# Kernel tuning notes

Hardware: AMD Instinct MI355X
Metric: run time of the kernel (lower is better)

## Reference

```python
import jax, jax.numpy as jnp
import numpy as np

HID, QLORA, NH = 5120, 1536, 128
NOPE, ROPE, KVLORA = 128, 64, 512
QHD = NOPE + ROPE  # 192
VHD = 128
SCALE = QHD ** (-0.5) * 0.707
EPS = 1e-6


def rmsnorm(x, w):
    xf = x.astype(jnp.float32)
    var = jnp.mean(xf * xf, axis=-1, keepdims=True)
    return (w * (xf * jax.lax.rsqrt(var + EPS))).astype(x.dtype)


def setup_inputs() -> dict:
    key = jax.random.key(0)
    ks = jax.random.split(key, 10)
    b, q, past = 2, 512, 512
    s = 0.02
    return {
        "hidden_states": jax.random.normal(ks[0], (b, q, HID), jnp.float32),
        "attention_mask": jnp.zeros((b, 1, q, past + q), jnp.float32),
        "past_key": jax.random.normal(ks[1], (b, NH, past, QHD), jnp.float32),
        "past_value": jax.random.normal(ks[2], (b, NH, past, VHD), jnp.float32),
        "w_q_a": jax.random.normal(ks[3], (QLORA, HID), jnp.float32) * s,
        "g_q_a": jnp.ones((QLORA,), jnp.float32),
        "w_q_b": jax.random.normal(ks[4], (NH * QHD, QLORA), jnp.float32) * s,
        "w_kv_a": jax.random.normal(ks[5], (KVLORA + ROPE, HID), jnp.float32) * s,
        "g_kv_a": jnp.ones((KVLORA,), jnp.float32),
        "w_kv_b": jax.random.normal(ks[6], (NH * (NOPE + VHD), KVLORA), jnp.float32) * s,
    }


def reference(hidden_states, attention_mask, past_key, past_value,
              w_q_a, g_q_a, w_q_b, w_kv_a, g_kv_a, w_kv_b):
    b, q_len, _ = hidden_states.shape
    # Q path: low-rank down-proj -> RMSNorm -> up-proj
    q = rmsnorm(hidden_states @ w_q_a.T, g_q_a) @ w_q_b.T
    q = q.reshape(b, q_len, NH, QHD).transpose(0, 2, 1, 3)  # [b,h,q,192]
    q_nope, q_pe = q[..., :NOPE], q[..., NOPE:]
    # KV path: joint down-proj, split latent / rope key
    ckv = hidden_states @ w_kv_a.T                          # [b,q,576]
    compressed_kv, k_pe = ckv[..., :KVLORA], ckv[..., KVLORA:]
    kv = rmsnorm(compressed_kv, g_kv_a) @ w_kv_b.T
    kv = kv.reshape(b, q_len, NH, NOPE + VHD).transpose(0, 2, 1, 3)
    k_nope, value_states = kv[..., :NOPE], kv[..., NOPE:]
    k_pe = k_pe.reshape(b, 1, q_len, ROPE)                  # shared across heads
    query_states = jnp.concatenate([q_nope, q_pe], axis=-1)
    key_states = jnp.concatenate(
        [k_nope, jnp.broadcast_to(k_pe, (b, NH, q_len, ROPE))], axis=-1)
    key_states = jnp.concatenate([past_key, key_states], axis=2)
    value_states = jnp.concatenate([past_value, value_states], axis=2)
    scores = jnp.einsum('bhqd,bhkd->bhqk', query_states, key_states) * SCALE
    scores = scores + attention_mask
    attn = jax.nn.softmax(scores.astype(jnp.float32), axis=-1).astype(query_states.dtype)
    attn_output = jnp.einsum('bhqk,bhkv->bhqv', attn, value_states)
    return attn_output, key_states, value_states
```

## Files before the change

kernel.cpp:

```cpp
#include <hip/hip_runtime.h>

#define NB    2
#define QLEN  512
#define HIDD  5120
#define QLORA 1536
#define NHEAD 128
#define QHD   192
#define VHD   128
#define KVTOT 1024

typedef float          f32x4   __attribute__((ext_vector_type(4)));
typedef __bf16         bf16x8  __attribute__((ext_vector_type(8)));
typedef unsigned short u16x8   __attribute__((ext_vector_type(8)));
typedef unsigned short u16x4   __attribute__((ext_vector_type(4)));

static __device__ __forceinline__ unsigned short f2bf(float f) {
  union { float f; unsigned u; } v; v.f = f;
  return (unsigned short)((v.u + 0x7fffu + ((v.u >> 16) & 1u)) >> 16);
}

static __device__ __forceinline__ void g2l16(const void* g, void* l) {
  __builtin_amdgcn_global_load_lds(
      (const __attribute__((address_space(1))) void*)g,
      (__attribute__((address_space(3))) void*)l, 16, 0, 0);
}

__global__ __launch_bounds__(256) void zero_pad_k(unsigned short* __restrict__ dst) {
  int i = blockIdx.x * 256 + threadIdx.x;
  u16x8 z = {0, 0, 0, 0, 0, 0, 0, 0};
  *(u16x8*)(dst + (long)i * 8) = z;
}

struct CvtArgs {
  const float* src[5];
  unsigned short* dst[5];
  int off[6];
};

__global__ __launch_bounds__(256) void cvt_all_k(CvtArgs a) {
  int b = blockIdx.x, s = 0;
  #pragma unroll
  for (int k = 0; k < 4; ++k) if (b >= a.off[k + 1]) s = k + 1;
  long lb = b - a.off[s];
  const float* in = a.src[s];
  unsigned short* out = a.dst[s];
  long base = lb * 1024 + threadIdx.x;
  #pragma unroll
  for (int k = 0; k < 4; ++k) {
    long i = base + k * 256;
    f32x4 v = *(const f32x4*)(in + i * 4);
    u16x4 o;
    o[0] = f2bf(v[0]); o[1] = f2bf(v[1]); o[2] = f2bf(v[2]); o[3] = f2bf(v[3]);
    *(u16x4*)(out + i * 4) = o;
  }
}

__global__ __launch_bounds__(256) void flags_k(const float* __restrict__ mask,
                                               int* __restrict__ flags) {
  int id = blockIdx.x;
  int b = id >> 6, qt = (id >> 4) & 3, kt = id & 15;
  const float* base = mask + (long)b * 524288 + (long)qt * 128 * 1024 + kt * 64;
  int t = threadIdx.x, w = t >> 6;
  unsigned acc = 0;
  #pragma unroll
  for (int i = 0; i < 32; ++i) {
    int e = i * 256 + t;
    int r = e >> 6, c = e & 63;
    union { float f; unsigned u; } v; v.f = base[(long)r * 1024 + c];
    acc |= v.u;
  }
  int any = __any(acc != 0);
  __shared__ int sf[4];
  if ((t & 63) == 0) sf[w] = any;
  __syncthreads();
  if (t == 0) flags[id] = sf[0] | sf[1] | sf[2] | sf[3];
}

__global__ __launch_bounds__(256, 4) void gemm_qa_ckv(const unsigned short* __restrict__ A,
                                                      const unsigned short* __restrict__ Bm,
                                                      float* __restrict__ part) {
  __shared__ __align__(16) unsigned short sA[128 * 64];
  __shared__ __align__(16) unsigned short sB[64 * 64];
  const int t = threadIdx.x, w = t >> 6, l = t & 63;
  const int l15 = l & 15, lh = l >> 4;
  const int swz7 = l15 & 7;
  const int id = blockIdx.x;
  const int xcd = id & 7, slot = id >> 3;
  const int pz = xcd + 8 * (slot >> 3);
  const int mb = slot & 7;
  if (pz >= 68) return;
  const int z = (pz >= 34) ? 1 : 0;
  const int nb = pz - z * 34;
  const unsigned short* Ab = A + (long)mb * 128 * HIDD;
  const unsigned short* Bb = Bm + (long)nb * 64 * HIDD;
  f32x4 acc[2][4];
  #pragma unroll
  for (int i = 0; i < 2; ++i)
    #pragma unroll
    for (int j = 0; j < 4; ++j)
      #pragma unroll
      for (int r = 0; r < 4; ++r) acc[i][j][r] = 0.f;

  const int k0 = z * 2560;
  for (int kt = k0; kt < k0 + 2560; kt += 64) {
    #pragma unroll
    for (int i2 = 0; i2 < 4; ++i2) {
      int n = i2 * 256 + t, r = n >> 3, c = (n & 7) ^ (r & 7);
      g2l16(Ab + (long)r * HIDD + kt + c * 8, (char*)sA + (i2 * 256 + w * 64) * 16);
    }
    #pragma unroll
    for (int i2 = 0; i2 < 2; ++i2) {
      int n = i2 * 256 + t, r = n >> 3, c = (n & 7) ^ (r & 7);
      g2l16(Bb + (long)r * HIDD + kt + c * 8, (char*)sB + (i2 * 256 + w * 64) * 16);
    }
    __syncthreads();
    #pragma unroll
    for (int ks = 0; ks < 2; ++ks) {
      bf16x8 af[2], bfr[4];
      #pragma unroll
      for (int i = 0; i < 2; ++i)
        af[i] = *(const bf16x8*)(sA + (w * 32 + i * 16 + l15) * 64 + ((ks * 4 + lh) ^ swz7) * 8);
      #pragma unroll
      for (int j = 0; j < 4; ++j)
        bfr[j] = *(const bf16x8*)(sB + (j * 16 + l15) * 64 + ((ks * 4 + lh) ^ swz7) * 8);
      #pragma unroll
      for (int i = 0; i < 2; ++i)
        #pragma unroll
        for (int j = 0; j < 4; ++j)
          acc[i][j] = __builtin_amdgcn_mfma_f32_16x16x32_bf16(af[i], bfr[j], acc[i][j], 0, 0, 0);
    }
    __syncthreads();
  }
  float* po = part + (long)z * 1024 * 2176;
  const int colbase = nb * 64;
  #pragma unroll
  for (int i = 0; i < 2; ++i)
    #pragma unroll
    for (int j = 0; j < 4; ++j) {
      const int col = colbase + j * 16 + l15;
      #pragma unroll
      for (int r4 = 0; r4 < 4; ++r4) {
        const long row = (long)mb * 128 + w * 32 + i * 16 + lh * 4 + r4;
        po[row * 2176 + col] = acc[i][j][r4];
      }
    }
}

__global__ __launch_bounds__(256) void post_a_k(const float* __restrict__ part,
                                                const float* __restrict__ gq,
                                                const float* __restrict__ gkv,
                                                unsigned short* __restrict__ qan,
                                                unsigned short* __restrict__ ckvn,
                                                float* __restrict__ kout,
                                                unsigned short* __restrict__ kb) {
  const long ZS = 1024L * 2176;
  int bid = blockIdx.x, t = threadIdx.x;
  if (bid >= 2048) {
    int row = bid - 2048;
    int j = t & 63, h0 = t >> 6;
    const float* p = part + (long)row * 2176 + 2048 + j;
    float v = p[0] + p[ZS];
    unsigned short vb = f2bf(v);
    long b_ = row >> 9, qi = row & 511;
    for (int h = h0; h < NHEAD; h += 4) {
      long idx = ((b_ * NHEAD + h) * KVTOT + 512 + qi) * QHD + 128 + j;
      kout[idx] = v;
      kb[idx] = vb;
    }
    return;
  }
  bool isQ = bid < 1024;
  int row = isQ ? bid : bid - 1024;
  int cols = isQ ? 1536 : 512;
  const float* g = isQ ? gq : gkv;
  unsigned short* out = isQ ? (qan + (long)row * 1536) : (ckvn + (long)row * 512);
  const float* x = part + (long)row * 2176 + (isQ ? 0 : 1536);
  int w = t >> 6, l = t & 63;
  float xv[6];
  int nc = cols >> 8;
  float ss = 0.f;
  for (int i = 0; i < nc; ++i) {
    int c = t + i * 256;
    float v = x[c] + x[c + ZS];
    xv[i] = v; ss += v * v;
  }
  #pragma unroll
  for (int m = 32; m >= 1; m >>= 1) ss += __shfl_xor(ss, m);
  __shared__ float red[4];
  if (l == 0) red[w] = ss;
  __syncthreads();
  float tot = red[0] + red[1] + red[2] + red[3];
  float rs = rsqrtf(tot / (float)cols + 1e-6f);
  for (int i = 0; i < nc; ++i) {
    int c = t + i * 256;
    out[c] = f2bf(g[c] * xv[i] * rs);
  }
}

__global__ __launch_bounds__(256, 4) void gemm_bt2(const unsigned short* __restrict__ Aq,
                                                   const unsigned short* __restrict__ Bq,
                                                   const unsigned short* __restrict__ Akv,
                                                   const unsigned short* __restrict__ Bkv,
                                                   unsigned short* __restrict__ qout,
                                                   float* __restrict__ kout,
                                                   float* __restrict__ vout,
                                                   unsigned short* __restrict__ kb,
                                                   unsigned short* __restrict__ vt) {
  __shared__ __align__(16) unsigned short sA[128 * 64];
  __shared__ __align__(16) unsigned short sB[128 * 64];
  const int t = threadIdx.x, w = t >> 6, l = t & 63;
  const int l15 = l & 15, lh = l >> 4;
  const int swz7 = l15 & 7;
  const int wm = w >> 1, wn = w & 1;
  const int id = blockIdx.x;
  const int xcd = id & 7, slot = id >> 3;
  const int y = xcd + 8 * (slot >> 3);
  const int mb = slot & 7;
  const bool isQ = y < 192;
  const int nb = isQ ? y : y - 192;
  const int K = isQ ? QLORA : 512;
  const unsigned short* Ab = (isQ ? Aq : Akv) + (long)mb * 128 * K;
  const unsigned short* Bb = (isQ ? Bq : Bkv) + (long)nb * 128 * K;
  f32x4 acc[4][4];
  #pragma unroll
  for (int i = 0; i < 4; ++i)
    #pragma unroll
    for (int j = 0; j < 4; ++j)
      #pragma unroll
      for (int r = 0; r < 4; ++r) acc[i][j][r] = 0.f;

  const int srow = l >> 3;
  const int scol = ((l & 7) ^ srow) * 8;

  for (int kt = 0; kt < K; kt += 64) {
    #pragma unroll
    for (int i = 0; i < 4; ++i) {
      const int chunk = i * 4 + w;
      const int r = chunk * 8 + srow;
      g2l16(Ab + (long)r * K + kt + scol, (char*)sA + chunk * 1024);
      g2l16(Bb + (long)r * K + kt + scol, (char*)sB + chunk * 1024);
    }
    __syncthreads();
    #pragma unroll
    for (int ks = 0; ks < 2; ++ks) {
      bf16x8 af[4], bfr[4];
      #pragma unroll
      for (int i = 0; i < 4; ++i)
        af[i] = *(const bf16x8*)(sA + (wm * 64 + i * 16 + l15) * 64 + ((ks * 4 + lh) ^ swz7) * 8);
      #pragma unroll
      for (int j = 0; j < 4; ++j)
        bfr[j] = *(const bf16x8*)(sB + (wn * 64 + j * 16 + l15) * 64 + ((ks * 4 + lh) ^ swz7) * 8);
      #pragma unroll
      for (int i = 0; i < 4; ++i)
        #pragma unroll
        for (int j = 0; j < 4; ++j)
          acc[i][j] = __builtin_amdgcn_mfma_f32_16x16x32_bf16(af[i], bfr[j], acc[i][j], 0, 0, 0);
    }
    __syncthreads();
  }

  const long rowbase = (long)mb * 128 + wm * 64;
  const long b_ = rowbase >> 9;
  const int colbase = nb * 128 + wn * 64;
  #pragma unroll
  for (int i = 0; i < 4; ++i) {
    const long qi0 = (rowbase + i * 16 + lh * 4) & 511;
    #pragma unroll
    for (int j = 0; j < 4; ++j) {
      const int col = colbase + j * 16 + l15;
      if (isQ) {
        const int h = col / QHD, d = col - h * QHD;
        unsigned short* qp = qout + ((b_ * NHEAD + h) * QLEN + qi0) * QHD + d;
        #pragma unroll
        for (int r4 = 0; r4 < 4; ++r4) qp[(long)r4 * QHD] = f2bf(acc[i][j][r4]);
      } else {
        const int h = col >> 8, d = col & 255;
        if (d < 128) {
          const long idx = ((b_ * NHEAD + h) * KVTOT + 512 + qi0) * QHD + d;
          #pragma unroll
          for (int r4 = 0; r4 < 4; ++r4) {
            kout[idx + (long)r4 * QHD] = acc[i][j][r4];
            kb[idx + (long)r4 * QHD] = f2bf(acc[i][j][r4]);
          }
        } else {
          const int dv = d - 128;
          float* vp = vout + ((b_ * NHEAD + h) * KVTOT + 512 + qi0) * VHD + dv;
          u16x4 tv;
          #pragma unroll
          for (int r4 = 0; r4 < 4; ++r4) {
            vp[(long)r4 * VHD] = acc[i][j][r4];
            tv[r4] = f2bf(acc[i][j][r4]);
          }
          *(u16x4*)(vt + ((b_ * NHEAD + h) * VHD + dv) * KVTOT + 512 + qi0) = tv;
        }
      }
    }
  }
}

__global__ __launch_bounds__(256) void copy_key_past_k(const float* __restrict__ pk,
                                                       float* __restrict__ kout,
                                                       unsigned short* __restrict__ kb) {
  long i4 = (long)blockIdx.x * 256 + threadIdx.x;
  f32x4 v = *(const f32x4*)(pk + i4 * 4);
  long e = i4 * 4;
  long bh = e / 98304;
  long rem = e - bh * 98304;
  long oidx = bh * 196608 + rem;
  *(f32x4*)(kout + oidx) = v;
  u16x4 b;
  b[0] = f2bf(v[0]); b[1] = f2bf(v[1]); b[2] = f2bf(v[2]); b[3] = f2bf(v[3]);
  *(u16x4*)(kb + oidx) = b;
}

__global__ __launch_bounds__(256) void vfix_k(const float* __restrict__ pv,
                                              float* __restrict__ outv,
                                              unsigned short* __restrict__ vt) {
  __shared__ __align__(16) unsigned short sT[128 * 72];
  int bh = blockIdx.x >> 3, kt = blockIdx.x & 7;
  int t = threadIdx.x;
  const float* src = pv + ((long)bh * 512 + kt * 64) * VHD;
  float* dstv = outv + ((long)bh * KVTOT + kt * 64) * VHD;
  #pragma unroll
  for (int i = 0; i < 8; ++i) {
    int id = t + i * 256;
    int r = id >> 5, c4 = (id & 31) * 4;
    f32x4 v = *(const f32x4*)(src + (long)r * VHD + c4);
    *(f32x4*)(dstv + (long)r * VHD + c4) = v;
    #pragma unroll
    for (int jj = 0; jj < 4; ++jj) sT[(c4 + jj) * 72 + r] = f2bf(v[jj]);
  }
  __syncthreads();
  #pragma unroll
  for (int i = 0; i < 4; ++i) {
    int id = t + i * 256;
    int d = id >> 3, c = id & 7;
    u16x8 v = *(const u16x8*)(sT + d * 72 + c * 8);
    *(u16x8*)(vt + ((long)bh * VHD + d) * KVTOT + kt * 64 + c * 8) = v;
  }
}

static __device__ __forceinline__ void stage_k_tile(const unsigned short* __restrict__ src,
                                                    char* dstbase, int t) {
  const int w = t >> 6;
  #pragma unroll
  for (int i2 = 0; i2 < 6; ++i2) {
    int n = i2 * 256 + t;
    int r = n / 24, cp = n - r * 24;
    int c = cp ^ (r & 7);
    g2l16(src + (long)r * QHD + c * 8, dstbase + (i2 * 256 + w * 64) * 16);
  }
}

static __device__ __forceinline__ void stage_v_tile(const unsigned short* __restrict__ src,
                                                    char* dstbase, int t) {
  const int w = t >> 6;
  #pragma unroll
  for (int i2 = 0; i2 < 4; ++i2) {
    int n = i2 * 256 + t;
    int r = n >> 3, cp = n & 7;
    int c = cp ^ (r & 7);
    g2l16(src + (long)r * KVTOT + c * 8, dstbase + (i2 * 256 + w * 64) * 16);
  }
}

__global__ __launch_bounds__(256, 2) void attn_k(const unsigned short* __restrict__ Qw,
                                                 const unsigned short* __restrict__ Kb,
                                                 const unsigned short* __restrict__ Vt,
                                                 const float* __restrict__ mask,
                                                 const int* __restrict__ flags,
                                                 float* __restrict__ outp) {
  __shared__ __align__(16) unsigned short sK[64 * 192];
  __shared__ __align__(16) unsigned short sV[128 * 64];
  const int t = threadIdx.x, w = t >> 6, l = t & 63;
  const int l15 = l & 15, lh = l >> 4;
  const int raw = blockIdx.x;
  const int xcd = raw & 7, slot = raw >> 3;
  const int bh = xcd * 32 + (slot >> 2), qt = slot & 3;
  const long b_ = bh >> 7;
  const float SCALE = 0.051023330039633184f;
  const int swz = l15 & 7;

  bf16x8 qf[2][6];
  const unsigned short* Qb = Qw + ((long)bh * QLEN + qt * 128 + w * 32) * QHD;
  #pragma unroll
  for (int i = 0; i < 2; ++i)
    #pragma unroll
    for (int ks = 0; ks < 6; ++ks)
      qf[i][ks] = *(const bf16x8*)(Qb + (i * 16 + l15) * QHD + ks * 32 + lh * 8);

  f32x4 o[2][8];
  #pragma unroll
  for (int i = 0; i < 2; ++i)
    #pragma unroll
    for (int j = 0; j < 8; ++j)
      #pragma unroll
      for (int r = 0; r < 4; ++r) o[i][j][r] = 0.f;
  float m_[2][4], l_[2][4];
  #pragma unroll
  for (int i = 0; i < 2; ++i)
    #pragma unroll
    for (int r = 0; r < 4; ++r) { m_[i][r] = -1e30f; l_[i][r] = 0.f; }

  const int qrow0 = qt * 128 + w * 32;
  const unsigned short* Kbh = Kb + (long)bh * KVTOT * QHD;
  const unsigned short* Vbh = Vt + (long)bh * VHD * KVTOT;
  const float* mrow = mask + b_ * 524288 + (long)(qrow0 + lh * 4) * 1024 + l15;
  const int fbase = (int)b_ * 64 + qt * 16;

  for (int kt = 0; kt < 16; ++kt) {
    stage_k_tile(Kbh + (long)kt * 64 * QHD, (char*)sK, t);
    stage_v_tile(Vbh + kt * 64, (char*)sV, t);
    const int flag = flags[fbase + kt];
    __syncthreads();

    f32x4 s[2][4];
    #pragma unroll
    for (int i = 0; i < 2; ++i)
      #pragma unroll
      for (int j = 0; j < 4; ++j)
        #pragma unroll
        for (int r = 0; r < 4; ++r) s[i][j][r] = 0.f;
    __builtin_amdgcn_s_setprio(1);
    #pragma unroll
    for (int j = 0; j < 4; ++j) {
      #pragma unroll
      for (int ks = 0; ks < 6; ++ks) {
        bf16x8 kf = *(const bf16x8*)(sK + ((j * 16 + l15) * 24 + ((ks * 4 + lh) ^ swz)) * 8);
        s[0][j] = __builtin_amdgcn_mfma_f32_16x16x32_bf16(qf[0][ks], kf, s[0][j], 0, 0, 0);
        s[1][j] = __builtin_amdgcn_mfma_f32_16x16x32_bf16(qf[1][ks], kf, s[1][j], 0, 0, 0);
      }
    }
    __builtin_amdgcn_s_setprio(0);

    unsigned short pk16[2][4][4];
    #pragma unroll
    for (int i = 0; i < 2; ++i) {
      #pragma unroll
      for (int rg = 0; rg < 4; ++rg) {
        float sc[4];
        if (flag) {
          #pragma unroll
          for (int j = 0; j < 4; ++j)
            sc[j] = s[i][j][rg] * SCALE + mrow[(long)(i * 16 + rg) * 1024 + kt * 64 + j * 16];
        } else {
          #pragma unroll
          for (int j = 0; j < 4; ++j) sc[j] = s[i][j][rg] * SCALE;
        }
        float mx = fmaxf(fmaxf(sc[0], sc[1]), fmaxf(sc[2], sc[3]));
        mx = fmaxf(mx, __shfl_xor(mx, 1));
        mx = fmaxf(mx, __shfl_xor(mx, 2));
        mx = fmaxf(mx, __shfl_xor(mx, 4));
        mx = fmaxf(mx, __shfl_xor(mx, 8));
        float mo = m_[i][rg];
        float mn = fmaxf(mo, mx);
        if (__any(mn > mo)) {
          float al = __expf(mo - mn);
          #pragma unroll
          for (int jj = 0; jj < 8; ++jj) o[i][jj][rg] *= al;
          l_[i][rg] *= al;
          m_[i][rg] = mn;
        }
        float ps = 0.f;
        #pragma unroll
        for (int j = 0; j < 4; ++j) {
          float p = __expf(sc[j] - m_[i][rg]);
          ps += p;
          pk16[i][rg][j] = f2bf(p);
        }
        l_[i][rg] += ps;
      }
    }
    __syncthreads();

    unsigned short* sPc = (unsigned short*)sK;
    #pragma unroll
    for (int i = 0; i < 2; ++i)
      #pragma unroll
      for (int rg = 0; rg < 4; ++rg) {
        const int prow = w * 32 + i * 16 + lh * 4 + rg;
        #pragma unroll
        for (int j = 0; j < 4; ++j)
          sPc[prow * 72 + j * 16 + l15] = pk16[i][rg][j];
      }

    __builtin_amdgcn_s_setprio(1);
    #pragma unroll
    for (int ks = 0; ks < 2; ++ks) {
      bf16x8 pf0 = *(const bf16x8*)(sPc + (w * 32 + l15) * 72 + ks * 32 + lh * 8);
      bf16x8 pf1 = *(const bf16x8*)(sPc + (w * 32 + 16 + l15) * 72 + ks * 32 + lh * 8);
      #pragma unroll
      for (int jj = 0; jj < 8; ++jj) {
        bf16x8 vf = *(const bf16x8*)(sV + ((jj * 16 + l15) * 8 + ((ks * 4 + lh) ^ swz)) * 8);
        o[0][jj] = __builtin_amdgcn_mfma_f32_16x16x32_bf16(pf0, vf, o[0][jj], 0, 0, 0);
        o[1][jj] = __builtin_amdgcn_mfma_f32_16x16x32_bf16(pf1, vf, o[1][jj], 0, 0, 0);
      }
    }
    __builtin_amdgcn_s_setprio(0);
    __syncthreads();
  }

  #pragma unroll
  for (int i = 0; i < 2; ++i) {
    #pragma unroll
    for (int rg = 0; rg < 4; ++rg) {
      float ls = l_[i][rg];
      ls += __shfl_xor(ls, 1);
      ls += __shfl_xor(ls, 2);
      ls += __shfl_xor(ls, 4);
      ls += __shfl_xor(ls, 8);
      float inv = 1.0f / ls;
      long row = (long)bh * QLEN + qrow0 + i * 16 + lh * 4 + rg;
      #pragma unroll
      for (int jj = 0; jj < 8; ++jj)
        outp[row * VHD + jj * 16 + l15] = o[i][jj][rg] * inv;
    }
  }
}

#define WS_HID_BF   0L
#define WS_WQA_BF   10485760L
#define WS_WQB_BF   32768000L
#define WS_WKVB_BF  108265472L
#define WS_QAN_BF   141819904L
#define WS_CKVN_BF  144965632L
#define WS_Q_BF     146014208L
#define WS_KB_BF    196345856L
#define WS_VT_BF    297009152L
#define WS_FLAGS    364118016L

extern "C" void kernel_launch(void* const* d_in, const int* in_sizes, int n_in,
                              void* d_out, int out_size, void* d_ws, size_t ws_size,
                              hipStream_t stream) {
  const float* hs   = (const float*)d_in[0];
  const float* mask = (const float*)d_in[1];
  const float* pk   = (const float*)d_in[2];
  const float* pv   = (const float*)d_in[3];
  const float* wqa  = (const float*)d_in[4];
  const float* gqa  = (const float*)d_in[5];
  const float* wqb  = (const float*)d_in[6];
  const float* wkva = (const float*)d_in[7];
  const float* gkva = (const float*)d_in[8];
  const float* wkvb = (const float*)d_in[9];

  char* ws = (char*)d_ws;
  unsigned short* hid_bf  = (unsigned short*)(ws + WS_HID_BF);
  unsigned short* wqa_bf  = (unsigned short*)(ws + WS_WQA_BF);
  unsigned short* wkva_bf = wqa_bf + (long)1536 * 5120;
  unsigned short* wpad_bf = wqa_bf + (long)2112 * 5120;
  unsigned short* wqb_bf  = (unsigned short*)(ws + WS_WQB_BF);
  unsigned short* wkvb_bf = (unsigned short*)(ws + WS_WKVB_BF);
  unsigned short* qan_bf  = (unsigned short*)(ws + WS_QAN_BF);
  unsigned short* ckvn_bf = (unsigned short*)(ws + WS_CKVN_BF);
  unsigned short* q_bf    = (unsigned short*)(ws + WS_Q_BF);
  float*          part    = (float*)(ws + WS_Q_BF);
  unsigned short* kb_bf   = (unsigned short*)(ws + WS_KB_BF);
  unsigned short* vt_bf   = (unsigned short*)(ws + WS_VT_BF);
  int*            flags   = (int*)(ws + WS_FLAGS);

  float* out_attn = (float*)d_out;
  float* out_key  = (float*)d_out + 16777216;
  float* out_val  = (float*)d_out + 67108864;

  flags_k<<<128, 256, 0, stream>>>(mask, flags);
  zero_pad_k<<<160, 256, 0, stream>>>(wpad_bf);
  CvtArgs ca;
  ca.src[0] = hs;     ca.dst[0] = hid_bf;
  ca.src[1] = wqa;    ca.dst[1] = wqa_bf;
  ca.src[2] = wkva;   ca.dst[2] = wkva_bf;
  ca.src[3] = wqb;    ca.dst[3] = wqb_bf;
  ca.src[4] = wkvb;   ca.dst[4] = wkvb_bf;
  ca.off[0] = 0; ca.off[1] = 1280; ca.off[2] = 3200; ca.off[3] = 3920;
  ca.off[4] = 13136; ca.off[5] = 17232;
  cvt_all_k<<<17232, 256, 0, stream>>>(ca);
  copy_key_past_k<<<24576, 256, 0, stream>>>(pk, out_key, kb_bf);
  gemm_qa_ckv<<<576, 256, 0, stream>>>(hid_bf, wqa_bf, part);
  post_a_k<<<3072, 256, 0, stream>>>(part, gqa, gkva, qan_bf, ckvn_bf, out_key, kb_bf);
  gemm_bt2<<<3584, 256, 0, stream>>>(qan_bf, wqb_bf, ckvn_bf, wkvb_bf,
                                     q_bf, out_key, out_val, kb_bf, vt_bf);
  vfix_k<<<2048, 256, 0, stream>>>(pv, out_val, vt_bf);
  attn_k<<<1024, 256, 0, stream>>>(q_bf, kb_bf, vt_bf, mask, flags, out_attn);
}
```

Before: 581.3 us.

## Merge prep kernels and overlap first GEMM with weight and past-KV conversion

Replaces flags, zero-pad and the first-stage conversions with a single prep kernel. A second combined kernel runs the q_a/ckv down-projection GEMM alongside the q_b/kv_b weight conversion, the past-key copy and the past-value copy/transpose by dispatching on block index. The goal is to cut launch overhead and fill idle CUs during the small 576-block GEMM with memory-bound copy work. In exchange, vfix now runs before gemm_bt2 instead of after, and the heterogeneous blocks share one launch config and LDS size.

Result: faster. 537.3 us (-7.6%).

```diff
diff --git a/kernel.cpp b/kernel.cpp
--- a/kernel.cpp
+++ b/kernel.cpp
@@ -25,125 +25,179 @@
       (__attribute__((address_space(3))) void*)l, 16, 0, 0);
 }
 
-__global__ __launch_bounds__(256) void zero_pad_k(unsigned short* __restrict__ dst) {
-  int i = blockIdx.x * 256 + threadIdx.x;
-  u16x8 z = {0, 0, 0, 0, 0, 0, 0, 0};
-  *(u16x8*)(dst + (long)i * 8) = z;
-}
-
-struct CvtArgs {
-  const float* src[5];
-  unsigned short* dst[5];
-  int off[6];
-};
-
-__global__ __launch_bounds__(256) void cvt_all_k(CvtArgs a) {
-  int b = blockIdx.x, s = 0;
-  #pragma unroll
-  for (int k = 0; k < 4; ++k) if (b >= a.off[k + 1]) s = k + 1;
-  long lb = b - a.off[s];
-  const float* in = a.src[s];
-  unsigned short* out = a.dst[s];
-  long base = lb * 1024 + threadIdx.x;
-  #pragma unroll
-  for (int k = 0; k < 4; ++k) {
-    long i = base + k * 256;
-    f32x4 v = *(const f32x4*)(in + i * 4);
-    u16x4 o;
-    o[0] = f2bf(v[0]); o[1] = f2bf(v[1]); o[2] = f2bf(v[2]); o[3] = f2bf(v[3]);
-    *(u16x4*)(out + i * 4) = o;
-  }
-}
-
-__global__ __launch_bounds__(256) void flags_k(const float* __restrict__ mask,
-                                               int* __restrict__ flags) {
-  int id = blockIdx.x;
-  int b = id >> 6, qt = (id >> 4) & 3, kt = id & 15;
-  const float* base = mask + (long)b * 524288 + (long)qt * 128 * 1024 + kt * 64;
-  int t = threadIdx.x, w = t >> 6;
-  unsigned acc = 0;
-  #pragma unroll
-  for (int i = 0; i < 32; ++i) {
-    int e = i * 256 + t;
-    int r = e >> 6, c = e & 63;
-    union { float f; unsigned u; } v; v.f = base[(long)r * 1024 + c];
-    acc |= v.u;
-  }
-  int any = __any(acc != 0);
+__global__ __launch_bounds__(256) void prep_k(const float* __restrict__ hs,
+                                              unsigned short* __restrict__ hid,
+                                              const float* __restrict__ wqa,
+                                              unsigned short* __restrict__ wqaB,
+                                              const float* __restrict__ wkva,
+                                              unsigned short* __restrict__ wkvaB,
+                                              const float* __restrict__ mask,
+                                              int* __restrict__ flags,
+                                              unsigned short* __restrict__ pad) {
   __shared__ int sf[4];
-  if ((t & 63) == 0) sf[w] = any;
-  __syncthreads();
-  if (t == 0) flags[id] = sf[0] | sf[1] | sf[2] | sf[3];
-}
-
-__global__ __launch_bounds__(256, 4) void gemm_qa_ckv(const unsigned short* __restrict__ A,
-                                                      const unsigned short* __restrict__ Bm,
-                                                      float* __restrict__ part) {
-  __shared__ __align__(16) unsigned short sA[128 * 64];
-  __shared__ __align__(16) unsigned short sB[64 * 64];
-  const int t = threadIdx.x, w = t >> 6, l = t & 63;
-  const int l15 = l & 15, lh = l >> 4;
-  const int swz7 = l15 & 7;
-  const int id = blockIdx.x;
-  const int xcd = id & 7, slot = id >> 3;
-  const int pz = xcd + 8 * (slot >> 3);
-  const int mb = slot & 7;
-  if (pz >= 68) return;
-  const int z = (pz >= 34) ? 1 : 0;
-  const int nb = pz - z * 34;
-  const unsigned short* Ab = A + (long)mb * 128 * HIDD;
-  const unsigned short* Bb = Bm + (long)nb * 64 * HIDD;
-  f32x4 acc[2][4];
-  #pragma unroll
-  for (int i = 0; i < 2; ++i)
-    #pragma unroll
-    for (int j = 0; j < 4; ++j)
-      #pragma unroll
-      for (int r = 0; r < 4; ++r) acc[i][j][r] = 0.f;
-
-  const int k0 = z * 2560;
-  for (int kt = k0; kt < k0 + 2560; kt += 64) {
-    #pragma unroll
-    for (int i2 = 0; i2 < 4; ++i2) {
-      int n = i2 * 256 + t, r = n >> 3, c = (n & 7) ^ (r & 7);
-      g2l16(Ab + (long)r * HIDD + kt + c * 8, (char*)sA + (i2 * 256 + w * 64) * 16);
-    }
-    #pragma unroll
-    for (int i2 = 0; i2 < 2; ++i2) {
-      int n = i2 * 256 + t, r = n >> 3, c = (n & 7) ^ (r & 7);
-      g2l16(Bb + (long)r * HIDD + kt + c * 8, (char*)sB + (i2 * 256 + w * 64) * 16);
-    }
-    __syncthreads();
-    #pragma unroll
-    for (int ks = 0; ks < 2; ++ks) {
-      bf16x8 af[2], bfr[4];
-      #pragma unroll
-      for (int i = 0; i < 2; ++i)
-        af[i] = *(const bf16x8*)(sA + (w * 32 + i * 16 + l15) * 64 + ((ks * 4 + lh) ^ swz7) * 8);
+  const int gid = blockIdx.x, t = threadIdx.x;
+  if (gid < 3920) {
+    const float* in; unsigned short* out; long lb;
+    if (gid < 1280)      { in = hs;   out = hid;   lb = gid; }
+    else if (gid < 3200) { in = wqa;  out = wqaB;  lb = gid - 1280; }
+    else                 { in = wkva; out = wkvaB; lb = gid - 3200; }
+    long base = lb * 1024 + t;
+    #pragma unroll
+    for (int k = 0; k < 4; ++k) {
+      long i = base + k * 256;
+      f32x4 v = *(const f32x4*)(in + i * 4);
+      u16x4 o;
+      o[0] = f2bf(v[0]); o[1] = f2bf(v[1]); o[2] = f2bf(v[2]); o[3] = f2bf(v[3]);
+      *(u16x4*)(out + i * 4) = o;
+    }
+  } else if (gid < 4048) {
+    int id = gid - 3920;
+    int b = id >> 6, qt = (id >> 4) & 3, kt = id & 15;
+    const float* base = mask + (long)b * 524288 + (long)qt * 128 * 1024 + kt * 64;
+    int w = t >> 6;
+    unsigned acc = 0;
+    #pragma unroll
+    for (int i = 0; i < 32; ++i) {
+      int e = i * 256 + t;
+      int r = e >> 6, c = e & 63;
+      union { float f; unsigned u; } v; v.f = base[(long)r * 1024 + c];
+      acc |= v.u;
+    }
+    int any = __any(acc != 0);
+    if ((t & 63) == 0) sf[w] = any;
+    __syncthreads();
+    if (t == 0) flags[id] = sf[0] | sf[1] | sf[2] | sf[3];
+  } else {
+    int i = (gid - 4048) * 256 + t;
+    u16x8 z = {0, 0, 0, 0, 0, 0, 0, 0};
+    *(u16x8*)(pad + (long)i * 8) = z;
+  }
+}
+
+__global__ __launch_bounds__(256, 4) void mega1_k(
+    const unsigned short* __restrict__ A, const unsigned short* __restrict__ Bm,
+    float* __restrict__ part,
+    const float* __restrict__ wqbF, unsigned short* __restrict__ wqbB,
+    const float* __restrict__ wkvbF, unsigned short* __restrict__ wkvbB,
+    const float* __restrict__ pk, float* __restrict__ kout, unsigned short* __restrict__ kb,
+    const float* __restrict__ pv, float* __restrict__ outv, unsigned short* __restrict__ vt) {
+  __shared__ __align__(16) char smem[24576];
+  const int gid = blockIdx.x, t = threadIdx.x;
+
+  if (gid < 576) {
+    unsigned short* sA = (unsigned short*)smem;
+    unsigned short* sB = (unsigned short*)(smem + 16384);
+    const int w = t >> 6, l = t & 63;
+    const int l15 = l & 15, lh = l >> 4;
+    const int swz7 = l15 & 7;
+    const int xcd = gid & 7, slot = gid >> 3;
+    const int pz = xcd + 8 * (slot >> 3);
+    const int mb = slot & 7;
+    if (pz >= 68) return;
+    const int z = (pz >= 34) ? 1 : 0;
+    const int nb = pz - z * 34;
+    const unsigned short* Ab = A + (long)mb * 128 * HIDD;
+    const unsigned short* Bb = Bm + (long)nb * 64 * HIDD;
+    f32x4 acc[2][4];
+    #pragma unroll
+    for (int i = 0; i < 2; ++i)
       #pragma unroll
       for (int j = 0; j < 4; ++j)
-        bfr[j] = *(const bf16x8*)(sB + (j * 16 + l15) * 64 + ((ks * 4 + lh) ^ swz7) * 8);
-      #pragma unroll
-      for (int i = 0; i < 2; ++i)
+        #pragma unroll
+        for (int r = 0; r < 4; ++r) acc[i][j][r] = 0.f;
+
+    const int k0 = z * 2560;
+    for (int kt = k0; kt < k0 + 2560; kt += 64) {
+      #pragma unroll
+      for (int i2 = 0; i2 < 4; ++i2) {
+        int n = i2 * 256 + t, r = n >> 3, c = (n & 7) ^ (r & 7);
+        g2l16(Ab + (long)r * HIDD + kt + c * 8, (char*)sA + (i2 * 256 + w * 64) * 16);
+      }
+      #pragma unroll
+      for (int i2 = 0; i2 < 2; ++i2) {
+        int n = i2 * 256 + t, r = n >> 3, c = (n & 7) ^ (r & 7);
+        g2l16(Bb + (long)r * HIDD + kt + c * 8, (char*)sB + (i2 * 256 + w * 64) * 16);
+      }
+      __syncthreads();
+      #pragma unroll
+      for (int ks = 0; ks < 2; ++ks) {
+        bf16x8 af[2], bfr[4];
+        #pragma unroll
+        for (int i = 0; i < 2; ++i)
+          af[i] = *(const bf16x8*)(sA + (w * 32 + i * 16 + l15) * 64 + ((ks * 4 + lh) ^ swz7) * 8);
         #pragma unroll
         for (int j = 0; j < 4; ++j)
-          acc[i][j] = __builtin_amdgcn_mfma_f32_16x16x32_bf16(af[i], bfr[j], acc[i][j], 0, 0, 0);
-    }
-    __syncthreads();
-  }
-  float* po = part + (long)z * 1024 * 2176;
-  const int colbase = nb * 64;
-  #pragma unroll
-  for (int i = 0; i < 2; ++i)
-    #pragma unroll
-    for (int j = 0; j < 4; ++j) {
-      const int col = colbase + j * 16 + l15;
-      #pragma unroll
-      for (int r4 = 0; r4 < 4; ++r4) {
-        const long row = (long)mb * 128 + w * 32 + i * 16 + lh * 4 + r4;
-        po[row * 2176 + col] = acc[i][j][r4];
-      }
-    }
+          bfr[j] = *(const bf16x8*)(sB + (j * 16 + l15) * 64 + ((ks * 4 + lh) ^ swz7) * 8);
+        #pragma unroll
+        for (int i = 0; i < 2; ++i)
+          #pragma unroll
+          for (int j = 0; j < 4; ++j)
+            acc[i][j] = __builtin_amdgcn_mfma_f32_16x16x32_bf16(af[i], bfr[j], acc[i][j], 0, 0, 0);
+      }
+      __syncthreads();
+    }
+    float* po = part + (long)z * 1024 * 2176;
+    const int colbase = nb * 64;
+    #pragma unroll
+    for (int i = 0; i < 2; ++i)
+      #pragma unroll
+      for (int j = 0; j < 4; ++j) {
+        const int col = colbase + j * 16 + l15;
+        #pragma unroll
+        for (int r4 = 0; r4 < 4; ++r4) {
+          const long row = (long)mb * 128 + w * 32 + i * 16 + lh * 4 + r4;
+          po[row * 2176 + col] = acc[i][j][r4];
+        }
+      }
+  } else if (gid < 13888) {
+    long lb = gid - 576;
+    const float* in; unsigned short* out;
+    if (lb < 9216) { in = wqbF; out = wqbB; }
+    else           { in = wkvbF; out = wkvbB; lb -= 9216; }
+    long base = lb * 1024 + t;
+    #pragma unroll
+    for (int k = 0; k < 4; ++k) {
+      long i = base + k * 256;
+      f32x4 v = *(const f32x4*)(in + i * 4);
+      u16x4 o;
+      o[0] = f2bf(v[0]); o[1] = f2bf(v[1]); o[2] = f2bf(v[2]); o[3] = f2bf(v[3]);
+      *(u16x4*)(out + i * 4) = o;
+    }
+  } else if (gid < 38464) {
+    long i4 = (long)(gid - 13888) * 256 + t;
+    f32x4 v = *(const f32x4*)(pk + i4 * 4);
+    long e = i4 * 4;
+    long bh = e / 98304;
+    long rem = e - bh * 98304;
+    long oidx = bh * 196608 + rem;
+    *(f32x4*)(kout + oidx) = v;
+    u16x4 b;
+    b[0] = f2bf(v[0]); b[1] = f2bf(v[1]); b[2] = f2bf(v[2]); b[3] = f2bf(v[3]);
+    *(u16x4*)(kb + oidx) = b;
+  } else {
+    unsigned short* sT = (unsigned short*)smem;
+    int lid = gid - 38464;
+    int bh = lid >> 3, kt = lid & 7;
+    const float* src = pv + ((long)bh * 512 + kt * 64) * VHD;
+    float* dstv = outv + ((long)bh * KVTOT + kt * 64) * VHD;
+    #pragma unroll
+    for (int i = 0; i < 8; ++i) {
+      int id = t + i * 256;
+      int r = id >> 5, c4 = (id & 31) * 4;
+      f32x4 v = *(const f32x4*)(src + (long)r * VHD + c4);
+      *(f32x4*)(dstv + (long)r * VHD + c4) = v;
+      #pragma unroll
+      for (int jj = 0; jj < 4; ++jj) sT[(c4 + jj) * 72 + r] = f2bf(v[jj]);
+    }
+    __syncthreads();
+    #pragma unroll
+    for (int i = 0; i < 4; ++i) {
+      int id = t + i * 256;
+      int d = id >> 3, c = id & 7;
+      u16x8 v = *(const u16x8*)(sT + d * 72 + c * 8);
+      *(u16x8*)(vt + ((long)bh * VHD + d) * KVTOT + kt * 64 + c * 8) = v;
+    }
+  }
 }
 
 __global__ __launch_bounds__(256) void post_a_k(const float* __restrict__ part,
@@ -298,48 +352,6 @@
   }
 }
 
-__global__ __launch_bounds__(256) void copy_key_past_k(const float* __restrict__ pk,
-                                                       float* __restrict__ kout,
-                                                       unsigned short* __restrict__ kb) {
-  long i4 = (long)blockIdx.x * 256 + threadIdx.x;
-  f32x4 v = *(const f32x4*)(pk + i4 * 4);
-  long e = i4 * 4;
-  long bh = e / 98304;
-  long rem = e - bh * 98304;
-  long oidx = bh * 196608 + rem;
-  *(f32x4*)(kout + oidx) = v;
-  u16x4 b;
-  b[0] = f2bf(v[0]); b[1] = f2bf(v[1]); b[2] = f2bf(v[2]); b[3] = f2bf(v[3]);
-  *(u16x4*)(kb + oidx) = b;
-}
-
-__global__ __launch_bounds__(256) void vfix_k(const float* __restrict__ pv,
-                                              float* __restrict__ outv,
-                                              unsigned short* __restrict__ vt) {
-  __shared__ __align__(16) unsigned short sT[128 * 72];
-  int bh = blockIdx.x >> 3, kt = blockIdx.x & 7;
-  int t = threadIdx.x;
-  const float* src = pv + ((long)bh * 512 + kt * 64) * VHD;
-  float* dstv = outv + ((long)bh * KVTOT + kt * 64) * VHD;
-  #pragma unroll
-  for (int i = 0; i < 8; ++i) {
-    int id = t + i * 256;
-    int r = id >> 5, c4 = (id & 31) * 4;
-    f32x4 v = *(const f32x4*)(src + (long)r * VHD + c4);
-    *(f32x4*)(dstv + (long)r * VHD + c4) = v;
-    #pragma unroll
-    for (int jj = 0; jj < 4; ++jj) sT[(c4 + jj) * 72 + r] = f2bf(v[jj]);
-  }
-  __syncthreads();
-  #pragma unroll
-  for (int i = 0; i < 4; ++i) {
-    int id = t + i * 256;
-    int d = id >> 3, c = id & 7;
-    u16x8 v = *(const u16x8*)(sT + d * 72 + c * 8);
-    *(u16x8*)(vt + ((long)bh * VHD + d) * KVTOT + kt * 64 + c * 8) = v;
-  }
-}
-
 static __device__ __forceinline__ void stage_k_tile(const unsigned short* __restrict__ src,
                                                     char* dstbase, int t) {
   const int w = t >> 6;
@@ -562,22 +574,14 @@
   float* out_key  = (float*)d_out + 16777216;
   float* out_val  = (float*)d_out + 67108864;
 
-  flags_k<<<128, 256, 0, stream>>>(mask, flags);
-  zero_pad_k<<<160, 256, 0, stream>>>(wpad_bf);
-  CvtArgs ca;
-  ca.src[0] = hs;     ca.dst[0] = hid_bf;
-  ca.src[1] = wqa;    ca.dst[1] = wqa_bf;
-  ca.src[2] = wkva;   ca.dst[2] = wkva_bf;
-  ca.src[3] = wqb;    ca.dst[3] = wqb_bf;
-  ca.src[4] = wkvb;   ca.dst[4] = wkvb_bf;
-  ca.off[0] = 0; ca.off[1] = 1280; ca.off[2] = 3200; ca.off[3] = 3920;
-  ca.off[4] = 13136; ca.off[5] = 17232;
-  cvt_all_k<<<17232, 256, 0, stream>>>(ca);
-  copy_key_past_k<<<24576, 256, 0, stream>>>(pk, out_key, kb_bf);
-  gemm_qa_ckv<<<576, 256, 0, stream>>>(hid_bf, wqa_bf, part);
+  prep_k<<<4208, 256, 0, stream>>>(hs, hid_bf, wqa, wqa_bf, wkva, wkva_bf,
+                                   mask, flags, wpad_bf);
+  mega1_k<<<40512, 256, 0, stream>>>(hid_bf, wqa_bf, part,
+                                     wqb, wqb_bf, wkvb, wkvb_bf,
+                                     pk, out_key, kb_bf,
+                                     pv, out_val, vt_bf);
   post_a_k<<<3072, 256, 0, stream>>>(part, gqa, gkva, qan_bf, ckvn_bf, out_key, kb_bf);
   gemm_bt2<<<3584, 256, 0, stream>>>(qan_bf, wqb_bf, ckvn_bf, wkvb_bf,
                                      q_bf, out_key, out_val, kb_bf, vt_bf);
-  vfix_k<<<2048, 256, 0, stream>>>(pv, out_val, vt_bf);
   attn_k<<<1024, 256, 0, stream>>>(q_bf, kb_bf, vt_bf, mask, flags, out_attn);
 }
```
